# Kernel optimization log

Measured on AMD Instinct MI355X. Metric: run time of the kernel, lower is better.

The kernel has to match this reference:

```python
import jax, jax.numpy as jnp
import numpy as np

# dims
B, N, C_A, C_S, C_Z = 2, 8192, 128, 384, 16
H, D = 4, 32            # n_heads, head_dim (H*D == C_A)
NQ, NK = 32, 128        # local window: queries / keys
NB = 3                  # n_blocks
W = N // NQ             # number of query windows
HID = 2 * C_A           # transition expansion (n=2)


def _ln(x, eps=1e-5):
    # LayerNorm without affine params
    m = jnp.mean(x, axis=-1, keepdims=True)
    v = jnp.var(x, axis=-1, keepdims=True)
    return (x - m) * jax.lax.rsqrt(v + eps)


def setup_inputs() -> dict:
    key = jax.random.key(0)
    ks = iter(jax.random.split(key, 40))
    def rn(shape, scale=1.0):
        return jax.random.normal(next(ks), shape, dtype=jnp.float32) * jnp.float32(scale)
    inp = {
        'q': rn((B, N, C_A)),
        's': rn((B, N, C_S)),
        'p': rn((B, W, NQ, NK, C_Z)),
        # AttentionPairBias (AF3 Alg 24) params, stacked over blocks
        'adaln_scale_w': rn((NB, C_S, C_A), C_S ** -0.5),
        'adaln_scale_b': jnp.zeros((NB, C_A), jnp.float32),
        'adaln_shift_w': rn((NB, C_S, C_A), C_S ** -0.5),
        'wq': rn((NB, C_A, H * D), C_A ** -0.5),
        'bq': jnp.zeros((NB, H * D), jnp.float32),
        'wk': rn((NB, C_A, H * D), C_A ** -0.5),
        'wv': rn((NB, C_A, H * D), C_A ** -0.5),
        'lnz_w': jnp.ones((NB, C_Z), jnp.float32),
        'lnz_b': jnp.zeros((NB, C_Z), jnp.float32),
        'wb_pair': rn((NB, C_Z, H), C_Z ** -0.5),
        'wg': rn((NB, C_A, H * D), C_A ** -0.5),
        'wo': rn((NB, H * D, C_A), (H * D) ** -0.5),
        'sgate_w': rn((NB, C_S, C_A), C_S ** -0.5),
        'sgate_b': jnp.full((NB, C_A), -2.0, jnp.float32),
        # ConditionedTransitionBlock (AF3 Alg 25) params
        't_scale_w': rn((NB, C_S, C_A), C_S ** -0.5),
        't_scale_b': jnp.zeros((NB, C_A), jnp.float32),
        't_shift_w': rn((NB, C_S, C_A), C_S ** -0.5),
        't_wa': rn((NB, C_A, HID), C_A ** -0.5),
        't_wb': rn((NB, C_A, HID), C_A ** -0.5),
        't_wo': rn((NB, HID, C_A), HID ** -0.5),
        't_sgate_w': rn((NB, C_S, C_A), C_S ** -0.5),
        't_sgate_b': jnp.full((NB, C_A), -2.0, jnp.float32),
    }
    return inp


def reference(q, s, p,
              adaln_scale_w, adaln_scale_b, adaln_shift_w,
              wq, bq, wk, wv, lnz_w, lnz_b, wb_pair, wg, wo, sgate_w, sgate_b,
              t_scale_w, t_scale_b, t_shift_w, t_wa, t_wb, t_wo, t_sgate_w, t_sgate_b):
    a = q
    s_ln = _ln(s)  # [B, N, C_S], shared across blocks
    # local window key indices: window w covers queries [w*NQ, (w+1)*NQ), keys
    # are a centered NK-wide window -> offsets in [-(NK-NQ)//2, ...)
    off = (NK - NQ) // 2
    idx = jnp.arange(W)[:, None] * NQ - off + jnp.arange(NK)[None, :]  # [W, NK]
    valid = (idx >= 0) & (idx < N)
    idx_c = jnp.clip(idx, 0, N - 1)
    inv_sqrt_d = jnp.float32(1.0 / np.sqrt(D))
    NEG = jnp.float32(-1e9)

    for i in range(NB):
        # ---- AttentionPairBias (AdaLN-conditioned, pair-biased, gated) ----
        a_ln = _ln(a)
        a_ln = jax.nn.sigmoid(s_ln @ adaln_scale_w[i] + adaln_scale_b[i]) * a_ln \
               + s_ln @ adaln_shift_w[i]
        qh = (a_ln @ wq[i] + bq[i]).reshape(B, N, H, D)
        kh = (a_ln @ wk[i]).reshape(B, N, H, D)
        vh = (a_ln @ wv[i]).reshape(B, N, H, D)
        g = jax.nn.sigmoid(a_ln @ wg[i]).reshape(B, N, H, D)
        # pair bias from z: LN + linear to heads -> [B, W, NQ, NK, H]
        bias = (_ln(p) * lnz_w[i] + lnz_b[i]) @ wb_pair[i]
        qw = qh.reshape(B, W, NQ, H, D)
        kw = kh[:, idx_c]  # [B, W, NK, H, D]
        vw = vh[:, idx_c]
        logits = jnp.einsum('bwqhd,bwkhd->bwqkh', qw, kw) * inv_sqrt_d + bias
        logits = jnp.where(valid[None, :, None, :, None], logits, NEG)
        attn = jax.nn.softmax(logits, axis=3)
        ow = jnp.einsum('bwqkh,bwkhd->bwqhd', attn, vw)
        o = (g * ow.reshape(B, N, H, D)).reshape(B, N, H * D)
        attn_out = (o @ wo[i]) * jax.nn.sigmoid(s_ln @ sgate_w[i] + sgate_b[i])
        # ---- ConditionedTransitionBlock (SwiGLU, sigmoid-gated) ----
        t_ln = _ln(a)
        t_ln = jax.nn.sigmoid(s_ln @ t_scale_w[i] + t_scale_b[i]) * t_ln \
               + s_ln @ t_shift_w[i]
        hidden = jax.nn.silu(t_ln @ t_wa[i]) * (t_ln @ t_wb[i])
        trans_out = (hidden @ t_wo[i]) * jax.nn.sigmoid(s_ln @ t_sgate_w[i] + t_sgate_b[i])
        # AF3 Alg 23: a <- b + ConditionedTransitionBlock(a, s)
        a = attn_out + trans_out
    return a
```

## Files before the change

kernel.cpp:

```cpp
#include <hip/hip_runtime.h>
#include <hip/hip_bf16.h>
#include <cstddef>
#include <cstdint>

#define BB   2
#define NN   8192
#define CA   128
#define CS   384
#define CZ   16
#define HH   4
#define DD   32
#define NQW  32
#define NKW  128
#define NBLK 3
#define WW   256
#define MR   (BB*NN)
#define HIDN 256

typedef unsigned short u16;
typedef __attribute__((ext_vector_type(8))) short short8;
typedef __attribute__((ext_vector_type(4))) float floatx4;

__device__ __forceinline__ float sigmoidf_(float x) { return 1.f / (1.f + __expf(-x)); }

__device__ __forceinline__ u16 f2bf(float x) {
  unsigned u = __float_as_uint(x);
  unsigned r = (u + 0x7fffu + ((u >> 16) & 1u)) >> 16;
  return (u16)r;
}
__device__ __forceinline__ float bf2f(u16 u) {
  return __uint_as_float(((unsigned)u) << 16);
}

__device__ __forceinline__ void gload16(const u16* g, u16* l) {
  __builtin_amdgcn_global_load_lds(
      (const __attribute__((address_space(1))) unsigned int*)g,
      (__attribute__((address_space(3))) unsigned int*)l, 16, 0, 0);
}

__global__ __launch_bounds__(256) void ln_s_kernel(const float* __restrict__ s,
                                                   u16* __restrict__ s_ln_bf) {
  int row  = blockIdx.x * 4 + (threadIdx.x >> 6);
  int lane = threadIdx.x & 63;
  const float* sr = s + (size_t)row * CS;
  float x[6];
  float sum = 0.f, sq = 0.f;
#pragma unroll
  for (int t = 0; t < 6; ++t) { x[t] = sr[lane + 64*t]; sum += x[t]; sq += x[t]*x[t]; }
#pragma unroll
  for (int off = 32; off; off >>= 1) { sum += __shfl_down(sum, off); sq += __shfl_down(sq, off); }
  sum = __shfl(sum, 0); sq = __shfl(sq, 0);
  float mean = sum * (1.f/CS);
  float var  = sq  * (1.f/CS) - mean*mean;
  float rstd = rsqrtf(var + 1e-5f);
  u16* orow = s_ln_bf + (size_t)row * CS;
#pragma unroll
  for (int t = 0; t < 6; ++t) orow[lane + 64*t] = f2bf((x[t]-mean)*rstd);
}

__global__ __launch_bounds__(256) void modln_kernel(const float* __restrict__ a,
                                                    const u16* __restrict__ sp0,
                                                    const u16* __restrict__ sp1,
                                                    const u16* __restrict__ sp3,
                                                    const u16* __restrict__ sp4,
                                                    u16* __restrict__ amod,
                                                    u16* __restrict__ tmod) {
  int row  = blockIdx.x * 4 + (threadIdx.x >> 6);
  int lane = threadIdx.x & 63;
  const float* ar = a + (size_t)row * CA;
  float x0 = ar[lane], x1 = ar[lane + 64];
  float sum = x0 + x1, sq = x0*x0 + x1*x1;
#pragma unroll
  for (int off = 32; off; off >>= 1) { sum += __shfl_down(sum, off); sq += __shfl_down(sq, off); }
  sum = __shfl(sum, 0); sq = __shfl(sq, 0);
  float mean = sum * (1.f/CA);
  float var  = sq  * (1.f/CA) - mean*mean;
  float rstd = rsqrtf(var + 1e-5f);
  float n0 = (x0-mean)*rstd, n1 = (x1-mean)*rstd;
  size_t i0 = (size_t)row * CA + lane;
  amod[i0]      = f2bf(bf2f(sp0[i0])     *n0 + bf2f(sp1[i0]));
  amod[i0 + 64] = f2bf(bf2f(sp0[i0 + 64])*n1 + bf2f(sp1[i0 + 64]));
  tmod[i0]      = f2bf(bf2f(sp3[i0])     *n0 + bf2f(sp4[i0]));
  tmod[i0 + 64] = f2bf(bf2f(sp3[i0 + 64])*n1 + bf2f(sp4[i0 + 64]));
}

struct TJob { const float* src; u16* dst; int K; int N; };
struct TJobs { TJob j[42]; };

__global__ __launch_bounds__(256) void transpose_bf16(TJobs jobs) {
  TJob jb = jobs.j[blockIdx.z];
  int tk = blockIdx.x * 32, tn = blockIdx.y * 32;
  if (tk >= jb.K || tn >= jb.N) return;
  __shared__ float tile[32][33];
  int tx = threadIdx.x & 31;
  int ty = threadIdx.x >> 5;
#pragma unroll
  for (int r = ty; r < 32; r += 8) tile[r][tx] = jb.src[(size_t)(tk + r) * jb.N + tn + tx];
  __syncthreads();
#pragma unroll
  for (int r = ty; r < 32; r += 8)
    jb.dst[(size_t)(tn + r) * jb.K + tk + tx] = f2bf(tile[tx][r]);
}

struct GemmJob {
  const u16* A;
  const u16* Bt;
  const u16* Bt2;
  const float* bias;
  u16* outbf;
  int K;
  int ostride;
  int mode;
  int pad;
};
struct GemmJobs { GemmJob j[18]; };

template <int NJ, int NX, bool DUAL>
__global__ __launch_bounds__(256) void gemm_mfma(GemmJobs jobs) {
  constexpr int NWG = NJ * NX * (MR / 128);
  const int lin = blockIdx.x;
  const int swz = (lin & 7) * (NWG >> 3) + (lin >> 3);
  const int job  = swz % NJ;
  const int rest = swz / NJ;
  const int bn = (rest % NX) * 128;
  const int bm = (rest / NX) * 128;

  GemmJob jb = jobs.j[job];
  const int K = jb.K;

  __shared__ u16 As[2][4096];
  __shared__ u16 Bs[2][4096];
  __shared__ u16 Bs2[DUAL ? 2 : 1][DUAL ? 4096 : 8];

  const int tid  = threadIdx.x;
  const int lane = tid & 63;
  const int wave = tid >> 6;
  const int wr = wave >> 1, wc = wave & 1;
  const int l15 = lane & 15, quad = lane >> 4;

  floatx4 acc[4][4] = {};
  floatx4 acc2[DUAL ? 4 : 1][DUAL ? 4 : 1] = {};

  const u16* Ab0  = jb.A  + ((size_t)bm + lane) * K + wave * 8;
  const u16* Ab1  = jb.A  + ((size_t)bm + 64 + lane) * K + wave * 8;
  const u16* Bb0  = jb.Bt + ((size_t)bn + lane) * K + wave * 8;
  const u16* Bb1  = jb.Bt + ((size_t)bn + 64 + lane) * K + wave * 8;
  const u16* B2b0 = DUAL ? (jb.Bt2 + ((size_t)bn + lane) * K + wave * 8) : nullptr;
  const u16* B2b1 = DUAL ? (jb.Bt2 + ((size_t)bn + 64 + lane) * K + wave * 8) : nullptr;

  auto stage = [&](int k0, int pb) {
    gload16(Ab0 + k0, As[pb] + wave * 1024);
    gload16(Ab1 + k0, As[pb] + wave * 1024 + 512);
    gload16(Bb0 + k0, Bs[pb] + wave * 1024);
    gload16(Bb1 + k0, Bs[pb] + wave * 1024 + 512);
    if constexpr (DUAL) {
      gload16(B2b0 + k0, Bs2[pb] + wave * 1024);
      gload16(B2b1 + k0, Bs2[pb] + wave * 1024 + 512);
    }
  };

  stage(0, 0);
  __syncthreads();
  int cur = 0;
  for (int k0 = 0; k0 < K; k0 += 32) {
    if (k0 + 32 < K) stage(k0 + 32, cur ^ 1);

    short8 a_frag[4], b_frag[4];
#pragma unroll
    for (int mt = 0; mt < 4; ++mt)
      a_frag[mt] = *(const short8*)(As[cur] + quad * 1024 + (wr * 64 + mt * 16 + l15) * 8);
#pragma unroll
    for (int nt = 0; nt < 4; ++nt)
      b_frag[nt] = *(const short8*)(Bs[cur] + quad * 1024 + (wc * 64 + nt * 16 + l15) * 8);
#pragma unroll
    for (int mt = 0; mt < 4; ++mt)
#pragma unroll
      for (int nt = 0; nt < 4; ++nt)
        acc[mt][nt] = __builtin_amdgcn_mfma_f32_16x16x32_bf16(a_frag[mt], b_frag[nt], acc[mt][nt], 0, 0, 0);
    if constexpr (DUAL) {
      short8 b2_frag[4];
#pragma unroll
      for (int nt = 0; nt < 4; ++nt)
        b2_frag[nt] = *(const short8*)(Bs2[cur] + quad * 1024 + (wc * 64 + nt * 16 + l15) * 8);
#pragma unroll
      for (int mt = 0; mt < 4; ++mt)
#pragma unroll
        for (int nt = 0; nt < 4; ++nt)
          acc2[mt][nt] = __builtin_amdgcn_mfma_f32_16x16x32_bf16(a_frag[mt], b2_frag[nt], acc2[mt][nt], 0, 0, 0);
    }
    __syncthreads();
    cur ^= 1;
  }

#pragma unroll
  for (int mt = 0; mt < 4; ++mt) {
#pragma unroll
    for (int nt = 0; nt < 4; ++nt) {
      int n = bn + wc * 64 + nt * 16 + l15;
      int mbase = bm + wr * 64 + mt * 16 + quad * 4;
      floatx4 v = acc[mt][nt];
      if constexpr (DUAL) {
        floatx4 v2 = acc2[mt][nt];
#pragma unroll
        for (int r = 0; r < 4; ++r) {
          size_t idx = (size_t)(mbase + r) * jb.ostride + n;
          float x1 = v[r];
          jb.outbf[idx] = f2bf(x1 * sigmoidf_(x1) * v2[r]);
        }
      } else if (jb.mode == 5) {
        int bidx = mbase >> 13;
        int tok  = mbase & (NN - 1);
        ushort4 o;
        o.x = f2bf(v[0]); o.y = f2bf(v[1]); o.z = f2bf(v[2]); o.w = f2bf(v[3]);
        *(ushort4*)(jb.outbf + (size_t)(bidx * CA + n) * NN + tok) = o;
      } else {
        float bias = jb.bias ? jb.bias[n] : 0.f;
#pragma unroll
        for (int r = 0; r < 4; ++r) {
          size_t idx = (size_t)(mbase + r) * jb.ostride + n;
          float x = v[r] + bias;
          jb.outbf[idx] = f2bf(jb.mode == 1 ? sigmoidf_(x) : x);
        }
      }
    }
  }
}

__global__ __launch_bounds__(256) void combo_kernel(const u16* __restrict__ O,
                                                    const u16* __restrict__ HID,
                                                    const u16* __restrict__ woT,
                                                    const u16* __restrict__ twoT,
                                                    const u16* __restrict__ g1,
                                                    const u16* __restrict__ g2,
                                                    float* __restrict__ outp) {
  const int bm = blockIdx.y * 64;
  __shared__ u16 As1[2][2048];
  __shared__ u16 Bs1[2][4096];
  __shared__ u16 As2[2][2048];
  __shared__ u16 Bs2h[2][4096];
  const int tid  = threadIdx.x;
  const int lane = tid & 63;
  const int wave = tid >> 6;
  const int wr = wave >> 1, wc = wave & 1;
  const int l15 = lane & 15, quad = lane >> 4;

  floatx4 acc1[2][4] = {};
  floatx4 acc2[2][4] = {};

  const u16* A1  = O    + ((size_t)bm + lane) * CA + wave * 8;
  const u16* B10 = woT  + ((size_t)lane) * CA + wave * 8;
  const u16* B11 = woT  + ((size_t)64 + lane) * CA + wave * 8;
  const u16* A2  = HID  + ((size_t)bm + lane) * HIDN + wave * 8;
  const u16* B20 = twoT + ((size_t)lane) * HIDN + wave * 8;
  const u16* B21 = twoT + ((size_t)64 + lane) * HIDN + wave * 8;

  auto stage1 = [&](int k0, int pb) {
    gload16(A1  + k0, As1[pb] + wave * 512);
    gload16(B10 + k0, Bs1[pb] + wave * 1024);
    gload16(B11 + k0, Bs1[pb] + wave * 1024 + 512);
  };
  auto stage2 = [&](int k0, int pb) {
    gload16(A2  + k0, As2[pb] + wave * 512);
    gload16(B20 + k0, Bs2h[pb] + wave * 1024);
    gload16(B21 + k0, Bs2h[pb] + wave * 1024 + 512);
  };

  stage1(0, 0);
  stage2(0, 0);
  __syncthreads();
  int cur = 0;
  for (int t = 0; t < 8; ++t) {
    if (t + 1 < 4) stage1((t + 1) * 32, cur ^ 1);
    if (t + 1 < 8) stage2((t + 1) * 32, cur ^ 1);

    if (t < 4) {
      short8 a_frag[2], b_frag[4];
#pragma unroll
      for (int mt = 0; mt < 2; ++mt)
        a_frag[mt] = *(const short8*)(As1[cur] + quad * 512 + (wr * 32 + mt * 16 + l15) * 8);
#pragma unroll
      for (int nt = 0; nt < 4; ++nt)
        b_frag[nt] = *(const short8*)(Bs1[cur] + quad * 1024 + (wc * 64 + nt * 16 + l15) * 8);
#pragma unroll
      for (int mt = 0; mt < 2; ++mt)
#pragma unroll
        for (int nt = 0; nt < 4; ++nt)
          acc1[mt][nt] = __builtin_amdgcn_mfma_f32_16x16x32_bf16(a_frag[mt], b_frag[nt], acc1[mt][nt], 0, 0, 0);
    }
    {
      short8 a_frag[2], b_frag[4];
#pragma unroll
      for (int mt = 0; mt < 2; ++mt)
        a_frag[mt] = *(const short8*)(As2[cur] + quad * 512 + (wr * 32 + mt * 16 + l15) * 8);
#pragma unroll
      for (int nt = 0; nt < 4; ++nt)
        b_frag[nt] = *(const short8*)(Bs2h[cur] + quad * 1024 + (wc * 64 + nt * 16 + l15) * 8);
#pragma unroll
      for (int mt = 0; mt < 2; ++mt)
#pragma unroll
        for (int nt = 0; nt < 4; ++nt)
          acc2[mt][nt] = __builtin_amdgcn_mfma_f32_16x16x32_bf16(a_frag[mt], b_frag[nt], acc2[mt][nt], 0, 0, 0);
    }
    __syncthreads();
    cur ^= 1;
  }

#pragma unroll
  for (int mt = 0; mt < 2; ++mt) {
#pragma unroll
    for (int nt = 0; nt < 4; ++nt) {
      int n = wc * 64 + nt * 16 + l15;
      int mbase = bm + wr * 32 + mt * 16 + quad * 4;
#pragma unroll
      for (int r = 0; r < 4; ++r) {
        size_t idx = (size_t)(mbase + r) * CA + n;
        outp[idx] = acc1[mt][nt][r] * bf2f(g1[idx]) + acc2[mt][nt][r] * bf2f(g2[idx]);
      }
    }
  }
}

__global__ __launch_bounds__(256) void bias3_kernel(const float* __restrict__ p,
                                                    const float* __restrict__ lnz_w,
                                                    const float* __restrict__ lnz_b,
                                                    const float* __restrict__ wb,
                                                    u16* __restrict__ biasT) {
  const int kc = blockIdx.x, w = blockIdx.y, b = blockIdx.z;
  __shared__ float effW[12][16];
  __shared__ float effb[12];
  const int t = threadIdx.x;
  if (t < 192) {
    int i = t >> 6, rem = t & 63, z = rem >> 2, hh = rem & 3;
    effW[i*4 + hh][z] = lnz_w[i*CZ + z] * wb[(i*CZ + z)*HH + hh];
  }
  if (t < 12) {
    int i = t >> 2, hh = t & 3;
    float acc = 0.f;
    for (int z = 0; z < 16; ++z) acc += lnz_b[i*CZ + z] * wb[(i*CZ + z)*HH + hh];
    effb[t] = acc;
  }
  __syncthreads();

  const int kk = t & 31, qg = (t >> 5) * 4;
  const int k = kc * 32 + kk;
  u16 out4[12][4];
#pragma unroll
  for (int r = 0; r < 4; ++r) {
    int qq = qg + r;
    const float4* pr = (const float4*)(p + (size_t)(((b * WW + w) * NQW + qq) * NKW + k) * 16);
    float4 p0 = pr[0], p1 = pr[1], p2 = pr[2], p3 = pr[3];
    float x[16] = {p0.x,p0.y,p0.z,p0.w, p1.x,p1.y,p1.z,p1.w,
                   p2.x,p2.y,p2.z,p2.w, p3.x,p3.y,p3.z,p3.w};
    float sum = 0.f, sq = 0.f;
#pragma unroll
    for (int z = 0; z < 16; ++z) { sum += x[z]; sq += x[z]*x[z]; }
    float mean = sum * (1.f/16.f);
    float var  = sq  * (1.f/16.f) - mean*mean;
    float rstd = rsqrtf(var + 1e-5f);
#pragma unroll
    for (int ih = 0; ih < 12; ++ih) {
      float acc = effb[ih];
#pragma unroll
      for (int z = 0; z < 16; ++z) acc += (x[z]-mean)*rstd * effW[ih][z];
      out4[ih][r] = f2bf(acc);
    }
  }
#pragma unroll
  for (int ih = 0; ih < 12; ++ih) {
    int i = ih >> 2, hh = ih & 3;
    u16* dst = biasT + ((((size_t)i * BB + b) * WW + w) * HH + hh) * 4096 + (size_t)k * 32 + qg;
    ushort4 uv; uv.x = out4[ih][0]; uv.y = out4[ih][1]; uv.z = out4[ih][2]; uv.w = out4[ih][3];
    *(ushort4*)dst = uv;
  }
}

__global__ __launch_bounds__(64) void attn_mfma(const u16* __restrict__ Qb,
                                                const u16* __restrict__ Kb,
                                                const u16* __restrict__ Vtb,
                                                const u16* __restrict__ Gb,
                                                const u16* __restrict__ biasT,
                                                u16* __restrict__ Ob) {
  const int w = blockIdx.x, h = blockIdx.y, b = blockIdx.z;
  __shared__ u16 Pt[128 * 36];
  __shared__ float inv_s[32];
  const int lane = threadIdx.x;
  const int l15 = lane & 15, quad = lane >> 4;
  const int tok0 = w * NQW - 48;

  short8 qf[2];
#pragma unroll
  for (int mt = 0; mt < 2; ++mt) {
    int qq = w * NQW + mt * 16 + l15;
    qf[mt] = *(const short8*)(Qb + (size_t)(b * NN + qq) * CA + h * DD + quad * 8);
  }
  floatx4 lg[2][8] = {};
#pragma unroll
  for (int nt = 0; nt < 8; ++nt) {
    int tk = tok0 + nt * 16 + l15;
    int tc = min(max(tk, 0), NN - 1);
    short8 kf = *(const short8*)(Kb + (size_t)(b * NN + tc) * CA + h * DD + quad * 8);
#pragma unroll
    for (int mt = 0; mt < 2; ++mt)
      lg[mt][nt] = __builtin_amdgcn_mfma_f32_16x16x32_bf16(qf[mt], kf, lg[mt][nt], 0, 0, 0);
  }

  const float scale = 0.17677669529663687f;
  const u16* bb = biasT + ((((size_t)b * WW + w) * HH + h) << 12);
  float mrow[2][4];
#pragma unroll
  for (int mt = 0; mt < 2; ++mt)
#pragma unroll
    for (int r = 0; r < 4; ++r) mrow[mt][r] = -3.0e38f;
#pragma unroll
  for (int nt = 0; nt < 8; ++nt) {
    int tk = tok0 + nt * 16 + l15;
    bool valid = (tk >= 0) && (tk < NN);
#pragma unroll
    for (int mt = 0; mt < 2; ++mt) {
      ushort4 bv = *(const ushort4*)(bb + (nt * 16 + l15) * 32 + mt * 16 + quad * 4);
      float bvf[4] = {bf2f(bv.x), bf2f(bv.y), bf2f(bv.z), bf2f(bv.w)};
#pragma unroll
      for (int r = 0; r < 4; ++r) {
        float l = valid ? (lg[mt][nt][r] * scale + bvf[r]) : -1e9f;
        lg[mt][nt][r] = l;
        mrow[mt][r] = fmaxf(mrow[mt][r], l);
      }
    }
  }
#pragma unroll
  for (int mt = 0; mt < 2; ++mt)
#pragma unroll
    for (int r = 0; r < 4; ++r) {
      float m = mrow[mt][r];
      m = fmaxf(m, __shfl_xor(m, 1));
      m = fmaxf(m, __shfl_xor(m, 2));
      m = fmaxf(m, __shfl_xor(m, 4));
      m = fmaxf(m, __shfl_xor(m, 8));
      mrow[mt][r] = m;
    }

  float srow[2][4] = {};
#pragma unroll
  for (int nt = 0; nt < 8; ++nt)
#pragma unroll
    for (int mt = 0; mt < 2; ++mt) {
      u16 pv[4];
#pragma unroll
      for (int r = 0; r < 4; ++r) {
        float e = __expf(lg[mt][nt][r] - mrow[mt][r]);
        srow[mt][r] += e;
        pv[r] = f2bf(e);
      }
      ushort4 uv; uv.x = pv[0]; uv.y = pv[1]; uv.z = pv[2]; uv.w = pv[3];
      *(ushort4*)(Pt + (nt * 16 + l15) * 36 + mt * 16 + quad * 4) = uv;
    }
#pragma unroll
  for (int mt = 0; mt < 2; ++mt)
#pragma unroll
    for (int r = 0; r < 4; ++r) {
      float ssum = srow[mt][r];
      ssum += __shfl_xor(ssum, 1);
      ssum += __shfl_xor(ssum, 2);
      ssum += __shfl_xor(ssum, 4);
      ssum += __shfl_xor(ssum, 8);
      if (l15 == 0) inv_s[mt * 16 + quad * 4 + r] = 1.f / ssum;
    }
  __syncthreads();

  floatx4 oacc[2][2] = {};
#pragma unroll
  for (int ks = 0; ks < 4; ++ks) {
    short8 pf[2];
#pragma unroll
    for (int ntq = 0; ntq < 2; ++ntq)
#pragma unroll
      for (int j = 0; j < 8; ++j)
        pf[ntq][j] = (short)Pt[(ks * 32 + quad * 8 + j) * 36 + ntq * 16 + l15];
    int tb = tok0 + ks * 32 + quad * 8;
    tb = min(max(tb, 0), NN - 8);
#pragma unroll
    for (int mtd = 0; mtd < 2; ++mtd) {
      short8 vf = *(const short8*)(Vtb + (size_t)(b * CA + h * DD + mtd * 16 + l15) * NN + tb);
#pragma unroll
      for (int ntq = 0; ntq < 2; ++ntq)
        oacc[mtd][ntq] = __builtin_amdgcn_mfma_f32_16x16x32_bf16(vf, pf[ntq], oacc[mtd][ntq], 0, 0, 0);
    }
  }

#pragma unroll
  for (int mtd = 0; mtd < 2; ++mtd)
#pragma unroll
    for (int ntq = 0; ntq < 2; ++ntq) {
      int qq = ntq * 16 + l15;
      float inv = inv_s[qq];
      int tok = w * NQW + qq;
      size_t base = (size_t)(b * NN + tok) * CA + h * DD + mtd * 16 + quad * 4;
      ushort4 gv = *(const ushort4*)(Gb + base);
      floatx4 v = oacc[mtd][ntq];
      ushort4 o;
      o.x = f2bf(bf2f(gv.x) * v[0] * inv);
      o.y = f2bf(bf2f(gv.y) * v[1] * inv);
      o.z = f2bf(bf2f(gv.z) * v[2] * inv);
      o.w = f2bf(bf2f(gv.w) * v[3] * inv);
      *(ushort4*)(Ob + base) = o;
    }
}

extern "C" void kernel_launch(void* const* d_in, const int* in_sizes, int n_in,
                              void* d_out, int out_size, void* d_ws, size_t ws_size,
                              hipStream_t stream) {
  const float* q             = (const float*)d_in[0];
  const float* s             = (const float*)d_in[1];
  const float* p             = (const float*)d_in[2];
  const float* adaln_scale_w = (const float*)d_in[3];
  const float* adaln_scale_b = (const float*)d_in[4];
  const float* adaln_shift_w = (const float*)d_in[5];
  const float* wq            = (const float*)d_in[6];
  const float* bq            = (const float*)d_in[7];
  const float* wk            = (const float*)d_in[8];
  const float* wv            = (const float*)d_in[9];
  const float* lnz_w         = (const float*)d_in[10];
  const float* lnz_b         = (const float*)d_in[11];
  const float* wb_pair       = (const float*)d_in[12];
  const float* wg            = (const float*)d_in[13];
  const float* wo            = (const float*)d_in[14];
  const float* sgate_w       = (const float*)d_in[15];
  const float* sgate_b       = (const float*)d_in[16];
  const float* t_scale_w     = (const float*)d_in[17];
  const float* t_scale_b     = (const float*)d_in[18];
  const float* t_shift_w     = (const float*)d_in[19];
  const float* t_wa          = (const float*)d_in[20];
  const float* t_wb          = (const float*)d_in[21];
  const float* t_wo          = (const float*)d_in[22];
  const float* t_sgate_w     = (const float*)d_in[23];
  const float* t_sgate_b     = (const float*)d_in[24];
  float* out = (float*)d_out;

  const size_t MC = (size_t)MR * CA;
  float* fws   = (float*)d_ws;
  float* abuf0 = fws;
  float* abuf1 = abuf0 + MC;
  u16* uws     = (u16*)(abuf1 + MC);
  u16* s_ln_bf = uws;
  u16* SP      = s_ln_bf + (size_t)MR * CS;
  u16* amod    = SP + 18*MC;
  u16* tmod    = amod + MC;
  u16* Qb      = tmod + MC;
  u16* Kb      = Qb + MC;
  u16* Vtb     = Kb + MC;
  u16* Gb      = Vtb + MC;
  u16* Ob      = Gb + MC;
  u16* HIDb    = Ob + MC;
  u16* biasT   = HIDb + 2*MC;
  u16* wbuf    = biasT + (size_t)3*BB*WW*HH*NQW*NKW;

  const size_t WBLK = 6*(size_t)CA*CS + 5*(size_t)CA*CA + 3*(size_t)CA*HIDN;
  const size_t o_ascale = 0;
  const size_t o_ashift = o_ascale + (size_t)CA*CS;
  const size_t o_sgate  = o_ashift + (size_t)CA*CS;
  const size_t o_tscale = o_sgate  + (size_t)CA*CS;
  const size_t o_tshift = o_tscale + (size_t)CA*CS;
  const size_t o_tsgate = o_tshift + (size_t)CA*CS;
  const size_t o_wq     = o_tsgate + (size_t)CA*CS;
  const size_t o_wk     = o_wq + (size_t)CA*CA;
  const size_t o_wv     = o_wk + (size_t)CA*CA;
  const size_t o_wg     = o_wv + (size_t)CA*CA;
  const size_t o_wo     = o_wg + (size_t)CA*CA;
  const size_t o_twa    = o_wo + (size_t)CA*CA;
  const size_t o_twb    = o_twa + (size_t)HIDN*CA;
  const size_t o_two    = o_twb + (size_t)HIDN*CA;

  ln_s_kernel<<<MR/4, 256, 0, stream>>>(s, s_ln_bf);

  TJobs tj;
  for (int i = 0; i < NBLK; ++i) {
    u16* wb0 = wbuf + (size_t)i * WBLK;
    int b14 = i * 14;
    tj.j[b14+0]  = TJob{adaln_scale_w + (size_t)i*CS*CA, wb0 + o_ascale, CS, CA};
    tj.j[b14+1]  = TJob{adaln_shift_w + (size_t)i*CS*CA, wb0 + o_ashift, CS, CA};
    tj.j[b14+2]  = TJob{sgate_w       + (size_t)i*CS*CA, wb0 + o_sgate,  CS, CA};
    tj.j[b14+3]  = TJob{t_scale_w     + (size_t)i*CS*CA, wb0 + o_tscale, CS, CA};
    tj.j[b14+4]  = TJob{t_shift_w     + (size_t)i*CS*CA, wb0 + o_tshift, CS, CA};
    tj.j[b14+5]  = TJob{t_sgate_w     + (size_t)i*CS*CA, wb0 + o_tsgate, CS, CA};
    tj.j[b14+6]  = TJob{wq   + (size_t)i*CA*CA,   wb0 + o_wq,  CA, CA};
    tj.j[b14+7]  = TJob{wk   + (size_t)i*CA*CA,   wb0 + o_wk,  CA, CA};
    tj.j[b14+8]  = TJob{wv   + (size_t)i*CA*CA,   wb0 + o_wv,  CA, CA};
    tj.j[b14+9]  = TJob{wg   + (size_t)i*CA*CA,   wb0 + o_wg,  CA, CA};
    tj.j[b14+10] = TJob{wo   + (size_t)i*CA*CA,   wb0 + o_wo,  CA, CA};
    tj.j[b14+11] = TJob{t_wa + (size_t)i*CA*HIDN, wb0 + o_twa, CA, HIDN};
    tj.j[b14+12] = TJob{t_wb + (size_t)i*CA*HIDN, wb0 + o_twb, CA, HIDN};
    tj.j[b14+13] = TJob{t_wo + (size_t)i*HIDN*CA, wb0 + o_two, HIDN, CA};
  }
  transpose_bf16<<<dim3(12, 8, 42), 256, 0, stream>>>(tj);

  bias3_kernel<<<dim3(4, WW, BB), 256, 0, stream>>>(p, lnz_w, lnz_b, wb_pair, biasT);

  {
    GemmJobs js = {};
    for (int i = 0; i < NBLK; ++i) {
      u16* wb0 = wbuf + (size_t)i * WBLK;
      js.j[i*6+0] = GemmJob{s_ln_bf, wb0 + o_ascale, nullptr, adaln_scale_b + i*CA, SP + (i*6+0)*MC, CS, CA, 1, 0};
      js.j[i*6+1] = GemmJob{s_ln_bf, wb0 + o_ashift, nullptr, nullptr,              SP + (i*6+1)*MC, CS, CA, 0, 0};
      js.j[i*6+2] = GemmJob{s_ln_bf, wb0 + o_sgate,  nullptr, sgate_b   + i*CA,     SP + (i*6+2)*MC, CS, CA, 1, 0};
      js.j[i*6+3] = GemmJob{s_ln_bf, wb0 + o_tscale, nullptr, t_scale_b + i*CA,     SP + (i*6+3)*MC, CS, CA, 1, 0};
      js.j[i*6+4] = GemmJob{s_ln_bf, wb0 + o_tshift, nullptr, nullptr,              SP + (i*6+4)*MC, CS, CA, 0, 0};
      js.j[i*6+5] = GemmJob{s_ln_bf, wb0 + o_tsgate, nullptr, t_sgate_b + i*CA,     SP + (i*6+5)*MC, CS, CA, 1, 0};
    }
    gemm_mfma<18, 1, false><<<18 * (MR/128), 256, 0, stream>>>(js);
  }

  for (int i = 0; i < NBLK; ++i) {
    const float* a_in = (i == 0) ? q : (i == 1 ? abuf0 : abuf1);
    float* a_out = (i == 2) ? out : (i == 0 ? abuf0 : abuf1);
    u16* wb0 = wbuf + (size_t)i * WBLK;

    modln_kernel<<<MR/4, 256, 0, stream>>>(a_in, SP + (i*6+0)*MC, SP + (i*6+1)*MC,
                                           SP + (i*6+3)*MC, SP + (i*6+4)*MC, amod, tmod);

    GemmJobs jq = {};
    jq.j[0] = GemmJob{amod, wb0 + o_wq, nullptr, bq + i*CA, Qb,  CA, CA, 0, 0};
    jq.j[1] = GemmJob{amod, wb0 + o_wk, nullptr, nullptr,   Kb,  CA, CA, 0, 0};
    jq.j[2] = GemmJob{amod, wb0 + o_wv, nullptr, nullptr,   Vtb, CA, CA, 5, 0};
    jq.j[3] = GemmJob{amod, wb0 + o_wg, nullptr, nullptr,   Gb,  CA, CA, 1, 0};
    gemm_mfma<4, 1, false><<<4 * (MR/128), 256, 0, stream>>>(jq);

    GemmJobs jh = {};
    jh.j[0] = GemmJob{tmod, wb0 + o_twa, wb0 + o_twb, nullptr, HIDb, CA, HIDN, 4, 0};
    gemm_mfma<1, 2, true><<<2 * (MR/128), 256, 0, stream>>>(jh);

    attn_mfma<<<dim3(WW, HH, BB), 64, 0, stream>>>(
        Qb, Kb, Vtb, Gb, biasT + (size_t)i * BB*WW*HH*4096, Ob);

    combo_kernel<<<dim3(1, MR/64), 256, 0, stream>>>(
        Ob, HIDb, wb0 + o_wo, wb0 + o_two,
        SP + (i*6+2)*MC, SP + (i*6+5)*MC, a_out);
  }
}
```

Before: 576.9 us.

## Triple-buffer GEMM smem with explicit vmcnt waits and drop block swizzle

New measurement: 573.1 us. No clear change (-0.7%).

```diff
diff --git a/kernel.cpp b/kernel.cpp
--- a/kernel.cpp
+++ b/kernel.cpp
@@ -115,22 +115,15 @@
 };
 struct GemmJobs { GemmJob j[18]; };
 
-template <int NJ, int NX, bool DUAL>
+template <bool DUAL>
 __global__ __launch_bounds__(256) void gemm_mfma(GemmJobs jobs) {
-  constexpr int NWG = NJ * NX * (MR / 128);
-  const int lin = blockIdx.x;
-  const int swz = (lin & 7) * (NWG >> 3) + (lin >> 3);
-  const int job  = swz % NJ;
-  const int rest = swz / NJ;
-  const int bn = (rest % NX) * 128;
-  const int bm = (rest / NX) * 128;
-
-  GemmJob jb = jobs.j[job];
+  GemmJob jb = jobs.j[blockIdx.z];
+  const int bm = blockIdx.y * 128, bn = blockIdx.x * 128;
   const int K = jb.K;
 
-  __shared__ u16 As[2][4096];
-  __shared__ u16 Bs[2][4096];
-  __shared__ u16 Bs2[DUAL ? 2 : 1][DUAL ? 4096 : 8];
+  __shared__ u16 As[3][4096];
+  __shared__ u16 Bs[3][4096];
+  __shared__ u16 Bs2[DUAL ? 3 : 1][DUAL ? 4096 : 8];
 
   const int tid  = threadIdx.x;
   const int lane = tid & 63;
@@ -159,19 +152,14 @@
     }
   };
 
-  stage(0, 0);
-  __syncthreads();
-  int cur = 0;
-  for (int k0 = 0; k0 < K; k0 += 32) {
-    if (k0 + 32 < K) stage(k0 + 32, cur ^ 1);
-
+  auto compute = [&](int pb) {
     short8 a_frag[4], b_frag[4];
 #pragma unroll
     for (int mt = 0; mt < 4; ++mt)
-      a_frag[mt] = *(const short8*)(As[cur] + quad * 1024 + (wr * 64 + mt * 16 + l15) * 8);
+      a_frag[mt] = *(const short8*)(As[pb] + quad * 1024 + (wr * 64 + mt * 16 + l15) * 8);
 #pragma unroll
     for (int nt = 0; nt < 4; ++nt)
-      b_frag[nt] = *(const short8*)(Bs[cur] + quad * 1024 + (wc * 64 + nt * 16 + l15) * 8);
+      b_frag[nt] = *(const short8*)(Bs[pb] + quad * 1024 + (wc * 64 + nt * 16 + l15) * 8);
 #pragma unroll
     for (int mt = 0; mt < 4; ++mt)
 #pragma unroll
@@ -181,16 +169,36 @@
       short8 b2_frag[4];
 #pragma unroll
       for (int nt = 0; nt < 4; ++nt)
-        b2_frag[nt] = *(const short8*)(Bs2[cur] + quad * 1024 + (wc * 64 + nt * 16 + l15) * 8);
+        b2_frag[nt] = *(const short8*)(Bs2[pb] + quad * 1024 + (wc * 64 + nt * 16 + l15) * 8);
 #pragma unroll
       for (int mt = 0; mt < 4; ++mt)
 #pragma unroll
         for (int nt = 0; nt < 4; ++nt)
           acc2[mt][nt] = __builtin_amdgcn_mfma_f32_16x16x32_bf16(a_frag[mt], b2_frag[nt], acc2[mt][nt], 0, 0, 0);
     }
-    __syncthreads();
-    cur ^= 1;
-  }
+  };
+
+  stage(0, 0);
+  stage(32, 1);
+  int cur = 0;
+  for (int k0 = 0; k0 + 64 < K; k0 += 32) {
+    stage(k0 + 64, (cur + 2) % 3);
+    if constexpr (DUAL) asm volatile("s_waitcnt vmcnt(12)" ::: "memory");
+    else                asm volatile("s_waitcnt vmcnt(8)"  ::: "memory");
+    __builtin_amdgcn_s_barrier();
+    compute(cur);
+    __builtin_amdgcn_s_barrier();
+    cur = (cur + 1) % 3;
+  }
+  if constexpr (DUAL) asm volatile("s_waitcnt vmcnt(6)" ::: "memory");
+  else                asm volatile("s_waitcnt vmcnt(4)" ::: "memory");
+  __builtin_amdgcn_s_barrier();
+  compute(cur);
+  __builtin_amdgcn_s_barrier();
+  cur = (cur + 1) % 3;
+  asm volatile("s_waitcnt vmcnt(0)" ::: "memory");
+  __builtin_amdgcn_s_barrier();
+  compute(cur);
 
 #pragma unroll
   for (int mt = 0; mt < 4; ++mt) {
@@ -606,7 +614,7 @@
       js.j[i*6+4] = GemmJob{s_ln_bf, wb0 + o_tshift, nullptr, nullptr,              SP + (i*6+4)*MC, CS, CA, 0, 0};
       js.j[i*6+5] = GemmJob{s_ln_bf, wb0 + o_tsgate, nullptr, t_sgate_b + i*CA,     SP + (i*6+5)*MC, CS, CA, 1, 0};
     }
-    gemm_mfma<18, 1, false><<<18 * (MR/128), 256, 0, stream>>>(js);
+    gemm_mfma<false><<<dim3(1, MR/128, 18), 256, 0, stream>>>(js);
   }
 
   for (int i = 0; i < NBLK; ++i) {
@@ -622,11 +630,11 @@
     jq.j[1] = GemmJob{amod, wb0 + o_wk, nullptr, nullptr,   Kb,  CA, CA, 0, 0};
     jq.j[2] = GemmJob{amod, wb0 + o_wv, nullptr, nullptr,   Vtb, CA, CA, 5, 0};
     jq.j[3] = GemmJob{amod, wb0 + o_wg, nullptr, nullptr,   Gb,  CA, CA, 1, 0};
-    gemm_mfma<4, 1, false><<<4 * (MR/128), 256, 0, stream>>>(jq);
+    gemm_mfma<false><<<dim3(1, MR/128, 4), 256, 0, stream>>>(jq);
 
     GemmJobs jh = {};
     jh.j[0] = GemmJob{tmod, wb0 + o_twa, wb0 + o_twb, nullptr, HIDb, CA, HIDN, 4, 0};
-    gemm_mfma<1, 2, true><<<2 * (MR/128), 256, 0, stream>>>(jh);
+    gemm_mfma<true><<<dim3(2, MR/128, 1), 256, 0, stream>>>(jh);
 
     attn_mfma<<<dim3(WW, HH, BB), 64, 0, stream>>>(
         Qb, Kb, Vtb, Gb, biasT + (size_t)i * BB*WW*HH*4096, Ob);
```
